# Performance work log

Hardware: AMD Instinct MI355X
Metric: run time of the kernel (lower is better)

## Reference

```python
import jax, jax.numpy as jnp
import numpy as np

BATCH = 16
D_MODEL = 384
STATE = 64          # state_dim
D_INNER = 384       # ssd_expand * d_model
H = 64
W = 64


def setup_inputs() -> dict:
    key = jax.random.key(0)
    ks = jax.random.split(key, 6)
    x = jax.random.normal(ks[0], (BATCH, D_MODEL, H * W), jnp.float32)
    # 1x1 Conv1d weights stored as 2D matrices [out_ch, in_ch]
    W_bcdt = jax.random.normal(ks[1], (3 * STATE, D_MODEL), jnp.float32) / np.sqrt(D_MODEL).astype(np.float32)
    # depthwise 3x3 conv, groups = 3*STATE -> kernel [3S, 1, 3, 3]
    W_dw = jax.random.normal(ks[2], (3 * STATE, 1, 3, 3), jnp.float32) / 3.0
    W_hz = jax.random.normal(ks[3], (2 * D_INNER, D_MODEL), jnp.float32) / np.sqrt(D_MODEL).astype(np.float32)
    W_out = jax.random.normal(ks[4], (D_MODEL, D_INNER), jnp.float32) / np.sqrt(D_INNER).astype(np.float32)
    A_param = jax.random.uniform(ks[5], (STATE,), jnp.float32, 1.0, 16.0)
    D_param = jnp.ones((1,), jnp.float32)
    return {"x": x, "W_bcdt": W_bcdt, "W_dw": W_dw, "W_hz": W_hz,
            "W_out": W_out, "A_param": A_param, "D_param": D_param,
            "size_h": H, "size_w": W}


def reference(x, W_bcdt, W_dw, W_hz, W_out, A_param, D_param, size_h, size_w):
    b, d, L = x.shape
    S = A_param.shape[0]
    # BCdt_proj: 1x1 conv1d == matmul over channel dim -> [b, 3S, L]
    bcdt = jnp.einsum('od,bdl->bol', W_bcdt, x)
    # depthwise 3x3 conv over the spatial view [b, 3S, H, W]
    xhw = bcdt.reshape(b, 3 * S, size_h, size_w)
    xhw = jax.lax.conv_general_dilated(
        xhw, W_dw, window_strides=(1, 1), padding='SAME',
        dimension_numbers=('NCHW', 'OIHW', 'NCHW'),
        feature_group_count=3 * S)
    bcdt = xhw.reshape(b, 3 * S, L)
    Bm, Cm, dt = jnp.split(bcdt, 3, axis=1)          # each [b, S, L]
    # softmax over the sequence dim with learned A offset
    A = jax.nn.softmax(dt + A_param[None, :, None], axis=-1)
    AB = A * Bm                                       # [b, S, L]
    h = jnp.einsum('bdl,bsl->bds', x, AB)             # x @ AB^T -> [b, d, S]
    hz = jnp.einsum('od,bds->bos', W_hz, h)           # hz_proj -> [b, 2*d_inner, S]
    h1, z = jnp.split(hz, 2, axis=1)                  # each [b, d_inner, S]
    hgate = h1 * jax.nn.silu(z) + h1 * D_param[0]
    hout = jnp.einsum('oe,bes->bos', W_out, hgate)    # out_proj -> [b, d, S]
    y = jnp.einsum('bds,bsl->bdl', hout, Cm)          # h @ C -> [b, d, L]
    y = y.reshape(b, d, size_h, size_w)
    return (y, hout)
```

## Files before the change

### kernel.cpp

```cpp
#include <hip/hip_runtime.h>

typedef unsigned short u16;
typedef short s16x8 __attribute__((ext_vector_type(8)));
typedef float f32x4 __attribute__((ext_vector_type(4)));

#define NB 16
#define DMODEL 384
#define SDIM 64
#define LSEQ 4096
#define C3S 192

__device__ __forceinline__ float b2f(u16 u) {
    union { unsigned int i; float f; } v; v.i = ((unsigned int)u) << 16; return v.f;
}
__device__ __forceinline__ u16 f2b(float f) {
    union { float ff; unsigned int i; } v; v.ff = f;
    unsigned int x = v.i;
    unsigned int r = (x + 0x7fffu + ((x >> 16) & 1u)) >> 16;
    return (u16)r;
}

__global__ __launch_bounds__(512, 4) void k01_mfma(const float* __restrict__ x,
                                                   const float* __restrict__ Wb,
                                                   u16* __restrict__ rawb,
                                                   u16* __restrict__ xb) {
    __shared__ __align__(16) u16  XR[32 * 136];
    __shared__ __align__(16) short As[192 * 40];
    __shared__ __align__(16) short Bs[128 * 40];
    const int t = threadIdx.x;
    const int l0 = blockIdx.x * 128;
    const int b = blockIdx.y;
    const int lane = t & 63;
    const int w = t >> 6;
    const int wm = w >> 1, wn = w & 1;
    const int lm = lane & 15, kg = lane >> 4;

    f32x4 acc[3][4];
    #pragma unroll
    for (int i = 0; i < 3; ++i)
        #pragma unroll
        for (int j = 0; j < 4; ++j) acc[i][j] = (f32x4){0.f, 0.f, 0.f, 0.f};

    const int xr = t >> 4;
    const int xli = (t & 15) * 8;
    const int bl = t >> 2;
    const int bdq = (t & 3) * 8;

    for (int kc = 0; kc < DMODEL; kc += 32) {
        if (t < 192) {
            const float* wp = Wb + (size_t)t * DMODEL + kc;
            #pragma unroll
            for (int c = 0; c < 4; ++c) {
                float4 w0 = *reinterpret_cast<const float4*>(wp + c * 8);
                float4 w1 = *reinterpret_cast<const float4*>(wp + c * 8 + 4);
                s16x8 av;
                av[0] = (short)f2b(w0.x); av[1] = (short)f2b(w0.y); av[2] = (short)f2b(w0.z); av[3] = (short)f2b(w0.w);
                av[4] = (short)f2b(w1.x); av[5] = (short)f2b(w1.y); av[6] = (short)f2b(w1.z); av[7] = (short)f2b(w1.w);
                *reinterpret_cast<s16x8*>(&As[t * 40 + c * 8]) = av;
            }
        }
        {
            const size_t xoff = ((size_t)(b * DMODEL + kc + xr)) * LSEQ + l0 + xli;
            const float* xp = x + xoff;
            float4 x0 = *reinterpret_cast<const float4*>(xp);
            float4 x1 = *reinterpret_cast<const float4*>(xp + 4);
            s16x8 v;
            v[0] = (short)f2b(x0.x); v[1] = (short)f2b(x0.y); v[2] = (short)f2b(x0.z); v[3] = (short)f2b(x0.w);
            v[4] = (short)f2b(x1.x); v[5] = (short)f2b(x1.y); v[6] = (short)f2b(x1.z); v[7] = (short)f2b(x1.w);
            *reinterpret_cast<s16x8*>(&XR[xr * 136 + xli]) = v;
            *reinterpret_cast<s16x8*>(xb + xoff) = v;
        }
        __syncthreads();
        {
            s16x8 v;
            #pragma unroll
            for (int j = 0; j < 8; ++j) v[j] = (short)XR[(bdq + j) * 136 + bl];
            *reinterpret_cast<s16x8*>(&Bs[bl * 40 + bdq]) = v;
        }
        __syncthreads();
        s16x8 af[3], bf[4];
        #pragma unroll
        for (int i = 0; i < 3; ++i)
            af[i] = *reinterpret_cast<s16x8*>(&As[(wm * 48 + i * 16 + lm) * 40 + kg * 8]);
        #pragma unroll
        for (int j = 0; j < 4; ++j)
            bf[j] = *reinterpret_cast<s16x8*>(&Bs[(wn * 64 + j * 16 + lm) * 40 + kg * 8]);
        #pragma unroll
        for (int i = 0; i < 3; ++i)
            #pragma unroll
            for (int j = 0; j < 4; ++j)
                acc[i][j] = __builtin_amdgcn_mfma_f32_16x16x32_bf16(af[i], bf[j], acc[i][j], 0, 0, 0);
        __syncthreads();
    }
    #pragma unroll
    for (int i = 0; i < 3; ++i) {
        #pragma unroll
        for (int j = 0; j < 4; ++j) {
            #pragma unroll
            for (int r = 0; r < 4; ++r) {
                int o = wm * 48 + i * 16 + kg * 4 + r;
                int l = l0 + wn * 64 + j * 16 + lm;
                rawb[((size_t)b * C3S + o) * LSEQ + l] = f2b(acc[i][j][r]);
            }
        }
    }
}

__global__ __launch_bounds__(256) void k23_ab(const u16* __restrict__ rawb,
                                              const float* __restrict__ Wdw,
                                              const float* __restrict__ Ap,
                                              u16* __restrict__ AB,
                                              u16* __restrict__ CMB) {
    __shared__ __align__(16) u16 chB[LSEQ];
    __shared__ __align__(16) u16 chC[LSEQ];
    __shared__ __align__(16) u16 chT[LSEQ];
    __shared__ float red[4];
    const int t = threadIdx.x;
    const int s = blockIdx.x;
    const int b = blockIdx.y;
    const u16* rB = rawb + ((size_t)b * C3S + s) * LSEQ;
    const u16* rC = rawb + ((size_t)b * C3S + 64 + s) * LSEQ;
    const u16* rT = rawb + ((size_t)b * C3S + 128 + s) * LSEQ;
    #pragma unroll
    for (int i = 0; i < 2; ++i) {
        int c8 = (t + i * 256) * 8;
        *reinterpret_cast<s16x8*>(&chB[c8]) = *reinterpret_cast<const s16x8*>(rB + c8);
        *reinterpret_cast<s16x8*>(&chC[c8]) = *reinterpret_cast<const s16x8*>(rC + c8);
        *reinterpret_cast<s16x8*>(&chT[c8]) = *reinterpret_cast<const s16x8*>(rT + c8);
    }
    __syncthreads();
    float wB[9], wC[9], wT[9];
    #pragma unroll
    for (int k = 0; k < 9; ++k) {
        wB[k] = Wdw[s * 9 + k];
        wC[k] = Wdw[(64 + s) * 9 + k];
        wT[k] = Wdw[(128 + s) * 9 + k];
    }
    const float a = Ap[s];
    u16* cmp = CMB + ((size_t)b * SDIM + s) * LSEQ;
    float vB[16], vT[16];
    float m = -3.0e38f;
    #pragma unroll
    for (int i = 0; i < 16; ++i) {
        int idx = t + i * 256;
        int row = idx >> 6, col = idx & 63;
        float aB = 0.f, aC = 0.f, aT = 0.f;
        #pragma unroll
        for (int dy = -1; dy <= 1; ++dy) {
            int r = row + dy;
            if (r < 0 || r > 63) continue;
            #pragma unroll
            for (int dx = -1; dx <= 1; ++dx) {
                int cc = col + dx;
                if (cc < 0 || cc > 63) continue;
                int p = r * 64 + cc;
                int wi = (dy + 1) * 3 + (dx + 1);
                aB = fmaf(wB[wi], b2f(chB[p]), aB);
                aC = fmaf(wC[wi], b2f(chC[p]), aC);
                aT = fmaf(wT[wi], b2f(chT[p]), aT);
            }
        }
        cmp[idx] = f2b(aC);
        vB[i] = aB;
        vT[i] = aT + a;
        m = fmaxf(m, vT[i]);
    }
    #pragma unroll
    for (int off = 32; off; off >>= 1) m = fmaxf(m, __shfl_xor(m, off));
    if ((t & 63) == 0) red[t >> 6] = m;
    __syncthreads();
    m = fmaxf(fmaxf(red[0], red[1]), fmaxf(red[2], red[3]));
    __syncthreads();
    float sum = 0.f;
    #pragma unroll
    for (int i = 0; i < 16; ++i) {
        vT[i] = expf(vT[i] - m);
        sum += vT[i];
    }
    #pragma unroll
    for (int off = 32; off; off >>= 1) sum += __shfl_xor(sum, off);
    if ((t & 63) == 0) red[t >> 6] = sum;
    __syncthreads();
    sum = red[0] + red[1] + red[2] + red[3];
    const float inv = 1.0f / sum;
    u16* op = AB + ((size_t)b * SDIM + s) * LSEQ;
    #pragma unroll
    for (int i = 0; i < 16; ++i) {
        int idx = t + i * 256;
        op[idx] = f2b(vT[i] * inv * vB[i]);
    }
}

__global__ __launch_bounds__(256) void kcmT(const u16* __restrict__ CMB,
                                            u16* __restrict__ CmT) {
    __shared__ __align__(16) u16 T[64][72];
    const int t = threadIdx.x;
    const int l0 = blockIdx.x * 64;
    const int b = blockIdx.y;
    const int sr = t >> 2;
    const int lo = (t & 3) * 16;
    const u16* ip = CMB + ((size_t)(b * SDIM + sr)) * LSEQ + l0 + lo;
    s16x8 va = *reinterpret_cast<const s16x8*>(ip);
    s16x8 vb = *reinterpret_cast<const s16x8*>(ip + 8);
    *reinterpret_cast<s16x8*>(&T[sr][lo + 0]) = va;
    *reinterpret_cast<s16x8*>(&T[sr][lo + 8]) = vb;
    __syncthreads();
    const int lr = t >> 2;
    const int sof = (t & 3) * 16;
    s16x8 wa, wb;
    #pragma unroll
    for (int j = 0; j < 8; ++j) {
        wa[j] = (short)T[sof + j][lr];
        wb[j] = (short)T[sof + 8 + j][lr];
    }
    u16* op = CmT + ((size_t)(b * LSEQ + l0 + lr)) * SDIM + sof;
    *reinterpret_cast<s16x8*>(op + 0) = wa;
    *reinterpret_cast<s16x8*>(op + 8) = wb;
}

__global__ __launch_bounds__(256) void k4_mfma(const u16* __restrict__ xb,
                                               const u16* __restrict__ ABu,
                                               float* __restrict__ hpart) {
    __shared__ __align__(16) short As[32 * 40];
    __shared__ __align__(16) short Bs[64 * 40];
    const int t = threadIdx.x;
    const int d0 = blockIdx.x * 32;
    const int kc = blockIdx.y;
    const int b = blockIdx.z;
    const int lane = t & 63;
    const int w = t >> 6;
    const int wm = w >> 1, wn = w & 1;
    const int lm = lane & 15, kg = lane >> 4;
    const int arow = t >> 2;
    const int aoff = (t & 3) * 8;
    const u16* ap = xb + ((size_t)(b * DMODEL + d0 + (arow & 31))) * LSEQ + kc * 1024 + aoff;
    const u16* bp = ABu + ((size_t)(b * SDIM + arow)) * LSEQ + kc * 1024 + aoff;
    f32x4 acc[2];
    acc[0] = (f32x4){0.f, 0.f, 0.f, 0.f};
    acc[1] = (f32x4){0.f, 0.f, 0.f, 0.f};

    for (int ks = 0; ks < 1024; ks += 32) {
        if (t < 128) {
            s16x8 av = *reinterpret_cast<const s16x8*>(ap + ks);
            *reinterpret_cast<s16x8*>(&As[arow * 40 + aoff]) = av;
        }
        s16x8 bv = *reinterpret_cast<const s16x8*>(bp + ks);
        *reinterpret_cast<s16x8*>(&Bs[arow * 40 + aoff]) = bv;
        __syncthreads();
        s16x8 af = *reinterpret_cast<s16x8*>(&As[(wm * 16 + lm) * 40 + kg * 8]);
        s16x8 bf0 = *reinterpret_cast<s16x8*>(&Bs[(wn * 32 + lm) * 40 + kg * 8]);
        s16x8 bf1 = *reinterpret_cast<s16x8*>(&Bs[(wn * 32 + 16 + lm) * 40 + kg * 8]);
        acc[0] = __builtin_amdgcn_mfma_f32_16x16x32_bf16(af, bf0, acc[0], 0, 0, 0);
        acc[1] = __builtin_amdgcn_mfma_f32_16x16x32_bf16(af, bf1, acc[1], 0, 0, 0);
        __syncthreads();
    }
    #pragma unroll
    for (int j = 0; j < 2; ++j) {
        int d = d0 + wm * 16 + kg * 4;
        int s = wn * 32 + j * 16 + lm;
        float* p = hpart + (size_t)kc * (1024 * DMODEL) + ((size_t)b * 64 + s) * DMODEL + d;
        *reinterpret_cast<f32x4*>(p) = acc[j];
    }
}

__global__ __launch_bounds__(256) void k5hz(const float* __restrict__ HPART,
                                            const float* __restrict__ Whz,
                                            float* __restrict__ HZT) {
    __shared__ __align__(16) short As[64 * 40];
    __shared__ __align__(16) short Bs[64 * 40];
    const int t = threadIdx.x;
    const int m0 = blockIdx.x * 64;
    const int n0 = blockIdx.y * 64;
    const int lane = t & 63;
    const int w = t >> 6;
    const int wm = w >> 1, wn = w & 1;
    const int lm = lane & 15, kg = lane >> 4;
    const int arow = t >> 2;
    const int aoff = (t & 3) * 8;
    const int NPART = 1024 * DMODEL;
    const float* apg = HPART + (size_t)(m0 + arow) * DMODEL + aoff;
    const float* bpg = Whz + (size_t)(n0 + arow) * DMODEL + aoff;
    f32x4 acc[2][2];
    #pragma unroll
    for (int i = 0; i < 2; ++i)
        #pragma unroll
        for (int j = 0; j < 2; ++j) acc[i][j] = (f32x4){0.f, 0.f, 0.f, 0.f};

    for (int kc = 0; kc < DMODEL; kc += 32) {
        float4 s0 = make_float4(0.f, 0.f, 0.f, 0.f);
        float4 s1 = make_float4(0.f, 0.f, 0.f, 0.f);
        #pragma unroll
        for (int p = 0; p < 4; ++p) {
            float4 u0 = *reinterpret_cast<const float4*>(apg + (size_t)p * NPART + kc);
            float4 u1 = *reinterpret_cast<const float4*>(apg + (size_t)p * NPART + kc + 4);
            s0.x += u0.x; s0.y += u0.y; s0.z += u0.z; s0.w += u0.w;
            s1.x += u1.x; s1.y += u1.y; s1.z += u1.z; s1.w += u1.w;
        }
        s16x8 av;
        av[0] = (short)f2b(s0.x); av[1] = (short)f2b(s0.y); av[2] = (short)f2b(s0.z); av[3] = (short)f2b(s0.w);
        av[4] = (short)f2b(s1.x); av[5] = (short)f2b(s1.y); av[6] = (short)f2b(s1.z); av[7] = (short)f2b(s1.w);
        float4 b0 = *reinterpret_cast<const float4*>(bpg + kc);
        float4 b1 = *reinterpret_cast<const float4*>(bpg + kc + 4);
        s16x8 bv;
        bv[0] = (short)f2b(b0.x); bv[1] = (short)f2b(b0.y); bv[2] = (short)f2b(b0.z); bv[3] = (short)f2b(b0.w);
        bv[4] = (short)f2b(b1.x); bv[5] = (short)f2b(b1.y); bv[6] = (short)f2b(b1.z); bv[7] = (short)f2b(b1.w);
        *reinterpret_cast<s16x8*>(&As[arow * 40 + aoff]) = av;
        *reinterpret_cast<s16x8*>(&Bs[arow * 40 + aoff]) = bv;
        __syncthreads();
        s16x8 af[2], bf[2];
        #pragma unroll
        for (int i = 0; i < 2; ++i) {
            af[i] = *reinterpret_cast<s16x8*>(&As[(wm * 32 + i * 16 + lm) * 40 + kg * 8]);
            bf[i] = *reinterpret_cast<s16x8*>(&Bs[(wn * 32 + i * 16 + lm) * 40 + kg * 8]);
        }
        #pragma unroll
        for (int i = 0; i < 2; ++i)
            #pragma unroll
            for (int j = 0; j < 2; ++j)
                acc[i][j] = __builtin_amdgcn_mfma_f32_16x16x32_bf16(af[i], bf[j], acc[i][j], 0, 0, 0);
        __syncthreads();
    }
    #pragma unroll
    for (int i = 0; i < 2; ++i) {
        #pragma unroll
        for (int j = 0; j < 2; ++j) {
            #pragma unroll
            for (int r = 0; r < 4; ++r) {
                int bs = m0 + wm * 32 + i * 16 + kg * 4 + r;
                int o = n0 + wn * 32 + j * 16 + lm;
                HZT[(size_t)bs * 768 + o] = acc[i][j][r];
            }
        }
    }
}

__global__ __launch_bounds__(256) void k5ho(const float* __restrict__ HZT,
                                            const float* __restrict__ Wout,
                                            const float* __restrict__ Dp,
                                            float* __restrict__ ho,
                                            u16* __restrict__ hob) {
    __shared__ __align__(16) short As[64 * 40];
    __shared__ __align__(16) short Bs[64 * 40];
    const int t = threadIdx.x;
    const int m0 = blockIdx.x * 64;
    const int n0 = blockIdx.y * 64;
    const int lane = t & 63;
    const int w = t >> 6;
    const int wm = w >> 1, wn = w & 1;
    const int lm = lane & 15, kg = lane >> 4;
    const int arow = t >> 2;
    const int aoff = (t & 3) * 8;
    const float* hzp = HZT + (size_t)(m0 + arow) * 768 + aoff;
    const float* bpg = Wout + (size_t)(n0 + arow) * DMODEL + aoff;
    const float Dv = Dp[0];
    f32x4 acc[2][2];
    #pragma unroll
    for (int i = 0; i < 2; ++i)
        #pragma unroll
        for (int j = 0; j < 2; ++j) acc[i][j] = (f32x4){0.f, 0.f, 0.f, 0.f};

    for (int kc = 0; kc < DMODEL; kc += 32) {
        float4 h0 = *reinterpret_cast<const float4*>(hzp + kc);
        float4 h1 = *reinterpret_cast<const float4*>(hzp + kc + 4);
        float4 z0 = *reinterpret_cast<const float4*>(hzp + DMODEL + kc);
        float4 z1 = *reinterpret_cast<const float4*>(hzp + DMODEL + kc + 4);
        s16x8 av;
        av[0] = (short)f2b(h0.x * (z0.x / (1.f + expf(-z0.x)) + Dv));
        av[1] = (short)f2b(h0.y * (z0.y / (1.f + expf(-z0.y)) + Dv));
        av[2] = (short)f2b(h0.z * (z0.z / (1.f + expf(-z0.z)) + Dv));
        av[3] = (short)f2b(h0.w * (z0.w / (1.f + expf(-z0.w)) + Dv));
        av[4] = (short)f2b(h1.x * (z1.x / (1.f + expf(-z1.x)) + Dv));
        av[5] = (short)f2b(h1.y * (z1.y / (1.f + expf(-z1.y)) + Dv));
        av[6] = (short)f2b(h1.z * (z1.z / (1.f + expf(-z1.z)) + Dv));
        av[7] = (short)f2b(h1.w * (z1.w / (1.f + expf(-z1.w)) + Dv));
        float4 b0 = *reinterpret_cast<const float4*>(bpg + kc);
        float4 b1 = *reinterpret_cast<const float4*>(bpg + kc + 4);
        s16x8 bv;
        bv[0] = (short)f2b(b0.x); bv[1] = (short)f2b(b0.y); bv[2] = (short)f2b(b0.z); bv[3] = (short)f2b(b0.w);
        bv[4] = (short)f2b(b1.x); bv[5] = (short)f2b(b1.y); bv[6] = (short)f2b(b1.z); bv[7] = (short)f2b(b1.w);
        *reinterpret_cast<s16x8*>(&As[arow * 40 + aoff]) = av;
        *reinterpret_cast<s16x8*>(&Bs[arow * 40 + aoff]) = bv;
        __syncthreads();
        s16x8 af[2], bf[2];
        #pragma unroll
        for (int i = 0; i < 2; ++i) {
            af[i] = *reinterpret_cast<s16x8*>(&As[(wm * 32 + i * 16 + lm) * 40 + kg * 8]);
            bf[i] = *reinterpret_cast<s16x8*>(&Bs[(wn * 32 + i * 16 + lm) * 40 + kg * 8]);
        }
        #pragma unroll
        for (int i = 0; i < 2; ++i)
            #pragma unroll
            for (int j = 0; j < 2; ++j)
                acc[i][j] = __builtin_amdgcn_mfma_f32_16x16x32_bf16(af[i], bf[j], acc[i][j], 0, 0, 0);
        __syncthreads();
    }
    #pragma unroll
    for (int i = 0; i < 2; ++i) {
        #pragma unroll
        for (int j = 0; j < 2; ++j) {
            int bs = m0 + wm * 32 + i * 16 + kg * 4;
            int b = bs >> 6, s = bs & 63;
            int o = n0 + wn * 32 + j * 16 + lm;
            size_t idx = ((size_t)b * DMODEL + o) * SDIM + s;
            *reinterpret_cast<f32x4*>(ho + idx) = acc[i][j];
            ushort4 u;
            u.x = f2b(acc[i][j][0]); u.y = f2b(acc[i][j][1]);
            u.z = f2b(acc[i][j][2]); u.w = f2b(acc[i][j][3]);
            *reinterpret_cast<ushort4*>(hob + idx) = u;
        }
    }
}

__global__ __launch_bounds__(256) void k6_mfma(const u16* __restrict__ CmT,
                                               const u16* __restrict__ hob,
                                               float* __restrict__ y) {
    const int t = threadIdx.x;
    const int l0 = blockIdx.x * 128;
    const int d0 = blockIdx.y * 128;
    const int b = blockIdx.z;
    const int lane = t & 63;
    const int w = t >> 6;
    const int wm = w >> 1, wn = w & 1;
    const int lm = lane & 15, kg = lane >> 4;
    const u16* hp = hob + (size_t)b * DMODEL * SDIM;
    const u16* cp = CmT + (size_t)b * LSEQ * SDIM;
    s16x8 af[4][2], bf[4][2];
    #pragma unroll
    for (int i = 0; i < 4; ++i)
        #pragma unroll
        for (int ks = 0; ks < 2; ++ks)
            af[i][ks] = *reinterpret_cast<const s16x8*>(
                hp + (size_t)(d0 + wm * 64 + i * 16 + lm) * SDIM + ks * 32 + kg * 8);
    #pragma unroll
    for (int j = 0; j < 4; ++j)
        #pragma unroll
        for (int ks = 0; ks < 2; ++ks)
            bf[j][ks] = *reinterpret_cast<const s16x8*>(
                cp + (size_t)(l0 + wn * 64 + j * 16 + lm) * SDIM + ks * 32 + kg * 8);
    f32x4 acc[4][4];
    #pragma unroll
    for (int i = 0; i < 4; ++i)
        #pragma unroll
        for (int j = 0; j < 4; ++j) acc[i][j] = (f32x4){0.f, 0.f, 0.f, 0.f};
    #pragma unroll
    for (int ks = 0; ks < 2; ++ks)
        #pragma unroll
        for (int i = 0; i < 4; ++i)
            #pragma unroll
            for (int j = 0; j < 4; ++j)
                acc[i][j] = __builtin_amdgcn_mfma_f32_16x16x32_bf16(af[i][ks], bf[j][ks], acc[i][j], 0, 0, 0);
    float* yp = y + (size_t)b * DMODEL * LSEQ;
    #pragma unroll
    for (int i = 0; i < 4; ++i) {
        #pragma unroll
        for (int j = 0; j < 4; ++j) {
            #pragma unroll
            for (int r = 0; r < 4; ++r) {
                int d = d0 + wm * 64 + i * 16 + kg * 4 + r;
                int l = l0 + wn * 64 + j * 16 + lm;
                yp[(size_t)d * LSEQ + l] = acc[i][j][r];
            }
        }
    }
}

extern "C" void kernel_launch(void* const* d_in, const int* in_sizes, int n_in,
                              void* d_out, int out_size, void* d_ws, size_t ws_size,
                              hipStream_t stream) {
    const float* x    = (const float*)d_in[0];
    const float* Wb   = (const float*)d_in[1];
    const float* Wdw  = (const float*)d_in[2];
    const float* Whz  = (const float*)d_in[3];
    const float* Wout = (const float*)d_in[4];
    const float* Ap   = (const float*)d_in[5];
    const float* Dp   = (const float*)d_in[6];

    float* out = (float*)d_out;
    const size_t YSIZE = (size_t)NB * DMODEL * LSEQ;

    u16*   RAWB   = (u16*)out;
    u16*   XB     = (u16*)(out + 6291456);
    u16*   CMB    = (u16*)(out + 18874368);
    u16*   ABu    = (u16*)(out + 20971520);
    float* HPART  = out;
    float* HZT    = out + 1572864;
    float* HO     = out + YSIZE;
    u16*   CmT    = (u16*)d_ws;
    u16*   HOB    = (u16*)d_ws + 4194304;

    k01_mfma<<<dim3(32, NB), 512, 0, stream>>>(x, Wb, RAWB, XB);
    k23_ab  <<<dim3(SDIM, NB), 256, 0, stream>>>(RAWB, Wdw, Ap, ABu, CMB);
    kcmT    <<<dim3(64, NB), 256, 0, stream>>>(CMB, CmT);
    k4_mfma <<<dim3(12, 4, NB), 256, 0, stream>>>(XB, ABu, HPART);
    k5hz    <<<dim3(16, 12), 256, 0, stream>>>(HPART, Whz, HZT);
    k5ho    <<<dim3(16, 6), 256, 0, stream>>>(HZT, Wout, Dp, HO, HOB);
    k6_mfma <<<dim3(32, 3, NB), 256, 0, stream>>>(CmT, HOB, out);
}
```

Before: 145.8 us.

## Drop bf16 copy of x; convert x on the fly in k4 and restructure k01

The first projection kernel no longer writes a bf16 copy of x to global memory. The h-reduction kernel instead reads fp32 x directly and converts it to bf16 while staging into shared memory. k01 is also retiled to 64-wide L tiles with 256 threads, and each wave now loads and converts its weight fragments straight from global memory into registers instead of going through a shared-memory A tile. This removes a 50MB bf16 write and replaces the read of the bf16 copy with a read of fp32 x, which is twice the bytes, and the weights are now reloaded more often per block.

Measured after the change: 153.5 us. +5.3%, slower.

```diff
diff --git a/kernel.cpp b/kernel.cpp
--- a/kernel.cpp
+++ b/kernel.cpp
@@ -20,19 +20,16 @@
     return (u16)r;
 }
 
-__global__ __launch_bounds__(512, 4) void k01_mfma(const float* __restrict__ x,
-                                                   const float* __restrict__ Wb,
-                                                   u16* __restrict__ rawb,
-                                                   u16* __restrict__ xb) {
-    __shared__ __align__(16) u16  XR[32 * 136];
-    __shared__ __align__(16) short As[192 * 40];
-    __shared__ __align__(16) short Bs[128 * 40];
-    const int t = threadIdx.x;
-    const int l0 = blockIdx.x * 128;
+__global__ __launch_bounds__(256) void k01_mfma(const float* __restrict__ x,
+                                                const float* __restrict__ Wb,
+                                                u16* __restrict__ rawb) {
+    __shared__ __align__(16) u16  XR[32 * 72];
+    __shared__ __align__(16) short Bs[64 * 40];
+    const int t = threadIdx.x;
+    const int l0 = blockIdx.x * 64;
     const int b = blockIdx.y;
     const int lane = t & 63;
     const int w = t >> 6;
-    const int wm = w >> 1, wn = w & 1;
     const int lm = lane & 15, kg = lane >> 4;
 
     f32x4 acc[3][4];
@@ -41,50 +38,44 @@
         #pragma unroll
         for (int j = 0; j < 4; ++j) acc[i][j] = (f32x4){0.f, 0.f, 0.f, 0.f};
 
-    const int xr = t >> 4;
-    const int xli = (t & 15) * 8;
-    const int bl = t >> 2;
-    const int bdq = (t & 3) * 8;
+    const int xr = t >> 3;
+    const int xli = (t & 7) * 8;
+    const int bl = t & 63;
+    const int bdq = (t >> 6) * 8;
 
     for (int kc = 0; kc < DMODEL; kc += 32) {
-        if (t < 192) {
-            const float* wp = Wb + (size_t)t * DMODEL + kc;
-            #pragma unroll
-            for (int c = 0; c < 4; ++c) {
-                float4 w0 = *reinterpret_cast<const float4*>(wp + c * 8);
-                float4 w1 = *reinterpret_cast<const float4*>(wp + c * 8 + 4);
-                s16x8 av;
-                av[0] = (short)f2b(w0.x); av[1] = (short)f2b(w0.y); av[2] = (short)f2b(w0.z); av[3] = (short)f2b(w0.w);
-                av[4] = (short)f2b(w1.x); av[5] = (short)f2b(w1.y); av[6] = (short)f2b(w1.z); av[7] = (short)f2b(w1.w);
-                *reinterpret_cast<s16x8*>(&As[t * 40 + c * 8]) = av;
-            }
-        }
         {
-            const size_t xoff = ((size_t)(b * DMODEL + kc + xr)) * LSEQ + l0 + xli;
-            const float* xp = x + xoff;
+            const float* xp = x + ((size_t)(b * DMODEL + kc + xr)) * LSEQ + l0 + xli;
             float4 x0 = *reinterpret_cast<const float4*>(xp);
             float4 x1 = *reinterpret_cast<const float4*>(xp + 4);
             s16x8 v;
             v[0] = (short)f2b(x0.x); v[1] = (short)f2b(x0.y); v[2] = (short)f2b(x0.z); v[3] = (short)f2b(x0.w);
             v[4] = (short)f2b(x1.x); v[5] = (short)f2b(x1.y); v[6] = (short)f2b(x1.z); v[7] = (short)f2b(x1.w);
-            *reinterpret_cast<s16x8*>(&XR[xr * 136 + xli]) = v;
-            *reinterpret_cast<s16x8*>(xb + xoff) = v;
+            *reinterpret_cast<s16x8*>(&XR[xr * 72 + xli]) = v;
+        }
+        s16x8 af[3];
+        #pragma unroll
+        for (int i = 0; i < 3; ++i) {
+            const float* wp = Wb + (size_t)(w * 48 + i * 16 + lm) * DMODEL + kc + kg * 8;
+            float4 w0 = *reinterpret_cast<const float4*>(wp);
+            float4 w1 = *reinterpret_cast<const float4*>(wp + 4);
+            af[i][0] = (short)f2b(w0.x); af[i][1] = (short)f2b(w0.y);
+            af[i][2] = (short)f2b(w0.z); af[i][3] = (short)f2b(w0.w);
+            af[i][4] = (short)f2b(w1.x); af[i][5] = (short)f2b(w1.y);
+            af[i][6] = (short)f2b(w1.z); af[i][7] = (short)f2b(w1.w);
         }
         __syncthreads();
         {
             s16x8 v;
             #pragma unroll
-            for (int j = 0; j < 8; ++j) v[j] = (short)XR[(bdq + j) * 136 + bl];
+            for (int j = 0; j < 8; ++j) v[j] = (short)XR[(bdq + j) * 72 + bl];
             *reinterpret_cast<s16x8*>(&Bs[bl * 40 + bdq]) = v;
         }
         __syncthreads();
-        s16x8 af[3], bf[4];
-        #pragma unroll
-        for (int i = 0; i < 3; ++i)
-            af[i] = *reinterpret_cast<s16x8*>(&As[(wm * 48 + i * 16 + lm) * 40 + kg * 8]);
+        s16x8 bf[4];
         #pragma unroll
         for (int j = 0; j < 4; ++j)
-            bf[j] = *reinterpret_cast<s16x8*>(&Bs[(wn * 64 + j * 16 + lm) * 40 + kg * 8]);
+            bf[j] = *reinterpret_cast<s16x8*>(&Bs[(j * 16 + lm) * 40 + kg * 8]);
         #pragma unroll
         for (int i = 0; i < 3; ++i)
             #pragma unroll
@@ -98,8 +89,8 @@
         for (int j = 0; j < 4; ++j) {
             #pragma unroll
             for (int r = 0; r < 4; ++r) {
-                int o = wm * 48 + i * 16 + kg * 4 + r;
-                int l = l0 + wn * 64 + j * 16 + lm;
+                int o = w * 48 + i * 16 + kg * 4 + r;
+                int l = l0 + j * 16 + lm;
                 rawb[((size_t)b * C3S + o) * LSEQ + l] = f2b(acc[i][j][r]);
             }
         }
@@ -218,7 +209,7 @@
     *reinterpret_cast<s16x8*>(op + 8) = wb;
 }
 
-__global__ __launch_bounds__(256) void k4_mfma(const u16* __restrict__ xb,
+__global__ __launch_bounds__(256) void k4_mfma(const float* __restrict__ x,
                                                const u16* __restrict__ ABu,
                                                float* __restrict__ hpart) {
     __shared__ __align__(16) short As[32 * 40];
@@ -233,7 +224,7 @@
     const int lm = lane & 15, kg = lane >> 4;
     const int arow = t >> 2;
     const int aoff = (t & 3) * 8;
-    const u16* ap = xb + ((size_t)(b * DMODEL + d0 + (arow & 31))) * LSEQ + kc * 1024 + aoff;
+    const float* ap = x + ((size_t)(b * DMODEL + d0 + (arow & 31))) * LSEQ + kc * 1024 + aoff;
     const u16* bp = ABu + ((size_t)(b * SDIM + arow)) * LSEQ + kc * 1024 + aoff;
     f32x4 acc[2];
     acc[0] = (f32x4){0.f, 0.f, 0.f, 0.f};
@@ -241,7 +232,11 @@
 
     for (int ks = 0; ks < 1024; ks += 32) {
         if (t < 128) {
-            s16x8 av = *reinterpret_cast<const s16x8*>(ap + ks);
+            float4 a0 = *reinterpret_cast<const float4*>(ap + ks);
+            float4 a1 = *reinterpret_cast<const float4*>(ap + ks + 4);
+            s16x8 av;
+            av[0] = (short)f2b(a0.x); av[1] = (short)f2b(a0.y); av[2] = (short)f2b(a0.z); av[3] = (short)f2b(a0.w);
+            av[4] = (short)f2b(a1.x); av[5] = (short)f2b(a1.y); av[6] = (short)f2b(a1.z); av[7] = (short)f2b(a1.w);
             *reinterpret_cast<s16x8*>(&As[arow * 40 + aoff]) = av;
         }
         s16x8 bv = *reinterpret_cast<const s16x8*>(bp + ks);
@@ -479,7 +474,6 @@
     const size_t YSIZE = (size_t)NB * DMODEL * LSEQ;
 
     u16*   RAWB   = (u16*)out;
-    u16*   XB     = (u16*)(out + 6291456);
     u16*   CMB    = (u16*)(out + 18874368);
     u16*   ABu    = (u16*)(out + 20971520);
     float* HPART  = out;
@@ -488,10 +482,10 @@
     u16*   CmT    = (u16*)d_ws;
     u16*   HOB    = (u16*)d_ws + 4194304;
 
-    k01_mfma<<<dim3(32, NB), 512, 0, stream>>>(x, Wb, RAWB, XB);
+    k01_mfma<<<dim3(64, NB), 256, 0, stream>>>(x, Wb, RAWB);
     k23_ab  <<<dim3(SDIM, NB), 256, 0, stream>>>(RAWB, Wdw, Ap, ABu, CMB);
     kcmT    <<<dim3(64, NB), 256, 0, stream>>>(CMB, CmT);
-    k4_mfma <<<dim3(12, 4, NB), 256, 0, stream>>>(XB, ABu, HPART);
+    k4_mfma <<<dim3(12, 4, NB), 256, 0, stream>>>(x, ABu, HPART);
     k5hz    <<<dim3(16, 12), 256, 0, stream>>>(HPART, Whz, HZT);
     k5ho    <<<dim3(16, 6), 256, 0, stream>>>(HZT, Wout, Dp, HO, HOB);
     k6_mfma <<<dim3(32, 3, NB), 256, 0, stream>>>(CmT, HOB, out);
```
